# Kernel optimization log

Measured on AMD Instinct MI355X. Metric: run time of the kernel, lower is better.

The kernel has to match this reference:

```python
import jax, jax.numpy as jnp
import numpy as np
import math

INPUT_SIZE = 1024
OUTPUT_SIZE = 1024
QK_SIZE = 1024
B, S = 4, 2048


def setup_inputs() -> dict:
    key = jax.random.key(0)
    ks = jax.random.split(key, 7)
    scale = 1.0 / math.sqrt(INPUT_SIZE)
    return {
        "x": jax.random.normal(ks[0], (B, S, INPUT_SIZE), dtype=jnp.float32),
        "Wq": jax.random.uniform(ks[1], (QK_SIZE, INPUT_SIZE), minval=-scale, maxval=scale, dtype=jnp.float32),
        "bq": jax.random.uniform(ks[2], (QK_SIZE,), minval=-scale, maxval=scale, dtype=jnp.float32),
        "Wk": jax.random.uniform(ks[3], (QK_SIZE, INPUT_SIZE), minval=-scale, maxval=scale, dtype=jnp.float32),
        "bk": jax.random.uniform(ks[4], (QK_SIZE,), minval=-scale, maxval=scale, dtype=jnp.float32),
        "Wv": jax.random.uniform(ks[5], (OUTPUT_SIZE, INPUT_SIZE), minval=-scale, maxval=scale, dtype=jnp.float32),
        "bv": jax.random.uniform(ks[6], (OUTPUT_SIZE,), minval=-scale, maxval=scale, dtype=jnp.float32),
    }


def reference(x, Wq, bq, Wk, bk, Wv, bv):
    # torch Linear: y = x @ W.T + b
    q = jnp.einsum('bsd,ed->bse', x, Wq) + bq  # [B,S,QK]
    k = jnp.einsum('bsd,ed->bse', x, Wk) + bk  # [B,S,QK]
    v = jnp.einsum('bsd,ed->bse', x, Wv) + bv  # [B,S,OUT]
    inv_sqrt_d = 1.0 / math.sqrt(QK_SIZE)
    scores = jnp.einsum('bqe,bke->bqk', q, k) * inv_sqrt_d  # [B,S,S]
    attn = jax.nn.softmax(scores, axis=-1)
    return jnp.einsum('bqk,bko->bqo', attn, v)  # [B,S,OUT]
```

## Files before the change

### kernel.cpp

```cpp
#include <hip/hip_runtime.h>
#include <stdint.h>

typedef unsigned short u16;
typedef __attribute__((ext_vector_type(8))) __bf16 bf16x8;
typedef __attribute__((ext_vector_type(4))) float f32x4;

__device__ __forceinline__ u16 f2bf(float f) {
    union { float f; uint32_t u; } v; v.f = f;
    uint32_t r = (v.u + 0x7FFFu + ((v.u >> 16) & 1u)) >> 16;
    return (u16)r;
}

__device__ __forceinline__ void lds_fence() {
    __asm__ volatile("s_waitcnt lgkmcnt(0)" ::: "memory");
}

#define BARRIER() __asm__ volatile("s_barrier" ::: "memory")
#define VMW(N)    __asm__ volatile("s_waitcnt vmcnt(" #N ")" ::: "memory")
#define SCHEDB()  __builtin_amdgcn_sched_barrier(0)

template<int MODE>
__global__ __launch_bounds__(512, 2) void gemm8(
    const u16* __restrict__ A, const u16* __restrict__ Bt,
    const float* __restrict__ b0, const float* __restrict__ b1, const float* __restrict__ b2,
    u16* __restrict__ o0, u16* __restrict__ o1, u16* __restrict__ o2,
    float* __restrict__ o3, float* __restrict__ lsum,
    int M, int N, int K, long sA, long sB, long sC, float scale)
{
    extern __shared__ __align__(16) u16 smem[];

    const int t = threadIdx.x;
    const int lane = t & 63;
    const int wave = t >> 6;
    const int wm = wave >> 2;
    const int wn = wave & 3;

    const int id = blockIdx.x;
    const int xcd = id & 7;
    const int s = id >> 3;
    int bm, bn;
    long bz;
    if (MODE == 0) {
        bm = (xcd * 4 + (s & 3)) * 256;
        bn = (s >> 2) * 256;
        bz = 0;
    } else if (MODE == 2) {
        bz = xcd >> 1;
        bm = ((xcd & 1) * 4 + (s & 3)) * 256;
        bn = (s >> 2) * 256;
    } else {
        bz = xcd >> 1;
        bm = ((xcd & 1) * 4 + (s & 3)) * 256;
        bn = (s >> 2) * 256;
    }

    const u16* Ab = A + bz * sA;
    const u16* Bb = Bt + bz * sB;

    f32x4 acc[8][4];
#pragma unroll
    for (int i = 0; i < 8; ++i)
#pragma unroll
        for (int j = 0; j < 4; ++j)
            acc[i][j] = (f32x4){0.f, 0.f, 0.f, 0.f};

    const int trow = t >> 2;
    const int gcol = ((t & 3) * 8) ^ ((trow & 8) << 1);
    const u16* aRow = Ab + (long)(bm + trow) * K + gcol;
    const u16* bRow = Bb + (long)(bn + trow) * K + gcol;

    auto stage = [&](int buf, int kt, int h, int isB) {
        const u16* g = (isB ? bRow : aRow) + (long)(h * 128) * K + kt * 64;
        u16* d = smem + t * 8 + buf * 32768 + isB * 16384 + h * 8192;
#pragma unroll
        for (int l = 0; l < 2; ++l)
            __builtin_amdgcn_global_load_lds(
                (const __attribute__((address_space(1))) void*)(g + l * 32),
                (__attribute__((address_space(3))) void*)(d + l * 4096), 16, 0, 0);
    };

    const int fm = lane & 15;
    const int fcol = ((lane >> 4) * 8) ^ ((fm & 8) << 1);
    const int aB = wm * 8192 + fm * 32 + fcol;
    const int bB = 16384 + (wn >> 1) * 8192 + (wn & 1) * 2048 + fm * 32 + fcol;

    bf16x8 fa[4][2], fb0[2][2], fb1[2][2];

#define RD_A(BUF, MH) do { \
    _Pragma("unroll") for (int mi = 0; mi < 4; ++mi) \
    _Pragma("unroll") for (int kh = 0; kh < 2; ++kh) \
        fa[mi][kh] = *(const bf16x8*)&smem[(BUF)*32768 + aB + kh*4096 + (MH)*2048 + mi*512]; \
} while (0)

#define RD_B(BUF, NH, DST) do { \
    _Pragma("unroll") for (int ni = 0; ni < 2; ++ni) \
    _Pragma("unroll") for (int kh = 0; kh < 2; ++kh) \
        DST[ni][kh] = *(const bf16x8*)&smem[(BUF)*32768 + bB + kh*4096 + (NH)*1024 + ni*512]; \
} while (0)

#define QUAD(MH, NH, FB) do { \
    __builtin_amdgcn_s_setprio(1); \
    _Pragma("unroll") for (int mi = 0; mi < 4; ++mi) \
    _Pragma("unroll") for (int ni = 0; ni < 2; ++ni) \
    _Pragma("unroll") for (int kh = 0; kh < 2; ++kh) \
        acc[(MH)*4+mi][(NH)*2+ni] = __builtin_amdgcn_mfma_f32_16x16x32_bf16( \
            fa[mi][kh], FB[ni][kh], acc[(MH)*4+mi][(NH)*2+ni], 0, 0, 0); \
    __builtin_amdgcn_s_setprio(0); \
} while (0)

    const int NT = K >> 6;
    const int NI = NT >> 1;

    stage(0, 0, 0, 0); stage(0, 0, 1, 0); stage(0, 0, 0, 1); stage(0, 0, 1, 1);
    stage(1, 1, 0, 1); stage(1, 1, 0, 0);
    VMW(4);
    BARRIER();

    for (int i = 0; i < NI; ++i) {
        const int knext = 2 * i + 1;
        int ktc = 2 * i + 2; if (ktc >= NT) ktc -= NT;
        const int ktd = ktc + 1;

        RD_A(0, 0); RD_B(0, 0, fb0);
        stage(1, knext, 1, 0);
        BARRIER(); SCHEDB();
        QUAD(0, 0, fb0);
        BARRIER();
        RD_B(0, 1, fb1);
        stage(1, knext, 1, 1);
        BARRIER(); SCHEDB();
        QUAD(0, 1, fb1);
        BARRIER();
        RD_A(0, 1);
        stage(0, ktc, 0, 1);
        BARRIER(); SCHEDB();
        QUAD(1, 1, fb1);
        BARRIER();
        stage(0, ktc, 0, 0);
        BARRIER(); SCHEDB();
        QUAD(1, 0, fb0);
        VMW(4);
        BARRIER();
        RD_A(1, 0); RD_B(1, 0, fb0);
        stage(0, ktc, 1, 0);
        BARRIER(); SCHEDB();
        QUAD(0, 0, fb0);
        BARRIER();
        RD_B(1, 1, fb1);
        stage(0, ktc, 1, 1);
        BARRIER(); SCHEDB();
        QUAD(0, 1, fb1);
        BARRIER();
        RD_A(1, 1);
        stage(1, ktd, 0, 1);
        BARRIER(); SCHEDB();
        QUAD(1, 1, fb1);
        BARRIER();
        stage(1, ktd, 0, 0);
        BARRIER(); SCHEDB();
        QUAD(1, 0, fb0);
        VMW(4);
        BARRIER();
    }

    VMW(0);
    BARRIER();

    const int cm = (lane >> 4) * 4;
    const int cn = lane & 15;
    u16* Ew = smem + wave * 8192;
    const int gmb = bm + wm * 128;
    const int cnb = bn + wn * 64;

    if (MODE == 3) {
        float* Fw = (float*)Ew;
#pragma unroll
        for (int p = 0; p < 4; ++p) {
            if (p) lds_fence();
#pragma unroll
            for (int m2 = 0; m2 < 2; ++m2) {
                const int mi = p * 2 + m2;
#pragma unroll
                for (int ni = 0; ni < 4; ++ni)
#pragma unroll
                    for (int r = 0; r < 4; ++r)
                        Fw[(m2 * 16 + cm + r) * 68 + ni * 16 + cn] = acc[mi][ni][r];
            }
#pragma unroll
            for (int it = 0; it < 8; ++it) {
                const int row = it * 4 + (lane >> 4);
                const int c4 = cn * 4;
                f32x4 w = *(const f32x4*)&Fw[row * 68 + c4];
                const int gm = gmb + p * 32 + row;
                const float inv = __builtin_amdgcn_rcpf(lsum[bz * 2048 + gm]);
                w[0] *= inv; w[1] *= inv; w[2] *= inv; w[3] *= inv;
                *(f32x4*)&o3[bz * sC + (long)gm * N + cnb + c4] = w;
            }
        }
    } else if (MODE == 0 && (bn >> 10) == 2) {
        const int ebase = (bn & 1023) + wn * 64;
        float bb[4];
#pragma unroll
        for (int ni = 0; ni < 4; ++ni) bb[ni] = b2[ebase + ni * 16 + cn];
        const long bgi = gmb >> 11;
        const int sbase = gmb & 2047;
#pragma unroll
        for (int p = 0; p < 2; ++p) {
            if (p) lds_fence();
#pragma unroll
            for (int m4 = 0; m4 < 4; ++m4) {
                const int mi = p * 4 + m4;
#pragma unroll
                for (int ni = 0; ni < 4; ++ni) {
                    ushort4 pk;
                    pk.x = f2bf(acc[mi][ni][0] + bb[ni]);
                    pk.y = f2bf(acc[mi][ni][1] + bb[ni]);
                    pk.z = f2bf(acc[mi][ni][2] + bb[ni]);
                    pk.w = f2bf(acc[mi][ni][3] + bb[ni]);
                    *(ushort4*)&Ew[(ni * 16 + cn) * 72 + m4 * 16 + cm] = pk;
                }
            }
#pragma unroll
            for (int it = 0; it < 8; ++it) {
                const int e = it * 8 + (lane >> 3);
                const int s8 = (lane & 7) * 8;
                const uint4 w = *(const uint4*)&Ew[e * 72 + s8];
                *(uint4*)&o2[(((bgi << 10) + ebase + e) << 11) + sbase + p * 64 + s8] = w;
            }
        }
    } else if (MODE == 0) {
        const int sec = bn >> 10;
        u16* C = sec ? o1 : o0;
        const float* bias = sec ? b1 : b0;
        const int ncol0 = (bn & 1023) + wn * 64;
        float bb[4];
#pragma unroll
        for (int ni = 0; ni < 4; ++ni) bb[ni] = bias[ncol0 + ni * 16 + cn];
#pragma unroll
        for (int p = 0; p < 2; ++p) {
            if (p) lds_fence();
#pragma unroll
            for (int m4 = 0; m4 < 4; ++m4) {
                const int mi = p * 4 + m4;
#pragma unroll
                for (int ni = 0; ni < 4; ++ni)
#pragma unroll
                    for (int r = 0; r < 4; ++r)
                        Ew[(m4 * 16 + cm + r) * 72 + ni * 16 + cn] = f2bf(acc[mi][ni][r] + bb[ni]);
            }
#pragma unroll
            for (int it = 0; it < 8; ++it) {
                const int row = it * 8 + (lane >> 3);
                const int c8 = (lane & 7) * 8;
                const uint4 w = *(const uint4*)&Ew[row * 72 + c8];
                *(uint4*)&C[(long)(gmb + p * 64 + row) * 1024 + ncol0 + c8] = w;
            }
        }
    } else {
#pragma unroll
        for (int mi = 0; mi < 8; ++mi)
#pragma unroll
            for (int ni = 0; ni < 4; ++ni)
#pragma unroll
                for (int r = 0; r < 4; ++r)
                    acc[mi][ni][r] = __expf(acc[mi][ni][r] * scale);
#pragma unroll
        for (int mi = 0; mi < 8; ++mi) {
#pragma unroll
            for (int r = 0; r < 4; ++r) {
                float sm = acc[mi][0][r] + acc[mi][1][r] + acc[mi][2][r] + acc[mi][3][r];
                sm += __shfl_xor(sm, 1);
                sm += __shfl_xor(sm, 2);
                sm += __shfl_xor(sm, 4);
                sm += __shfl_xor(sm, 8);
                if (cn == 0)
                    atomicAdd(&lsum[bz * 2048 + gmb + mi * 16 + cm + r], sm);
            }
        }
#pragma unroll
        for (int p = 0; p < 2; ++p) {
            if (p) lds_fence();
#pragma unroll
            for (int m4 = 0; m4 < 4; ++m4) {
                const int mi = p * 4 + m4;
#pragma unroll
                for (int ni = 0; ni < 4; ++ni)
#pragma unroll
                    for (int r = 0; r < 4; ++r)
                        Ew[(m4 * 16 + cm + r) * 72 + ni * 16 + cn] = f2bf(acc[mi][ni][r]);
            }
#pragma unroll
            for (int it = 0; it < 8; ++it) {
                const int row = it * 8 + (lane >> 3);
                const int c8 = (lane & 7) * 8;
                const uint4 w = *(const uint4*)&Ew[row * 72 + c8];
                *(uint4*)&o0[bz * sC + (long)(gmb + p * 64 + row) * N + cnb + c8] = w;
            }
        }
    }
}

#undef RD_A
#undef RD_B
#undef QUAD

__global__ __launch_bounds__(256) void cvt_all(
    const float* __restrict__ x, const float* __restrict__ wq,
    const float* __restrict__ wk, const float* __restrict__ wv,
    u16* __restrict__ xb, u16* __restrict__ wb, float* __restrict__ lsum)
{
    const int b = blockIdx.x;
    if (b >= 11264) {
        const long i = (long)(b - 11264) * 1024 + threadIdx.x * 4;
        *(f32x4*)(lsum + i) = (f32x4){0.f, 0.f, 0.f, 0.f};
        return;
    }
    const float* src; u16* dst; long base;
    if (b < 8192)       { src = x;  dst = xb;             base = (long)b * 1024; }
    else if (b < 9216)  { src = wq; dst = wb;             base = (long)(b - 8192) * 1024; }
    else if (b < 10240) { src = wk; dst = wb + (1 << 20); base = (long)(b - 9216) * 1024; }
    else                { src = wv; dst = wb + (2 << 20); base = (long)(b - 10240) * 1024; }
    const long i = base + threadIdx.x * 4;
    const f32x4 f = *(const f32x4*)(src + i);
    ushort4 o;
    o.x = f2bf(f[0]); o.y = f2bf(f[1]); o.z = f2bf(f[2]); o.w = f2bf(f[3]);
    *(ushort4*)(dst + i) = o;
}

extern "C" void kernel_launch(void* const* d_in, const int* in_sizes, int n_in,
                              void* d_out, int out_size, void* d_ws, size_t ws_size,
                              hipStream_t stream) {
    const float* x  = (const float*)d_in[0];
    const float* Wq = (const float*)d_in[1];
    const float* bq = (const float*)d_in[2];
    const float* Wk = (const float*)d_in[3];
    const float* bk = (const float*)d_in[4];
    const float* Wv = (const float*)d_in[5];
    const float* bv = (const float*)d_in[6];
    float* out = (float*)d_out;

    const int B = 4, S = 2048, D = 1024, E = 1024;
    const int M = B * S;
    const size_t LDS = 131072;

    u16* xb  = (u16*)d_ws;
    u16* wb  = xb  + (size_t)M * D;
    u16* qb  = wb  + (size_t)3 * E * D;
    u16* kb  = qb  + (size_t)M * E;
    u16* vbT = kb  + (size_t)M * E;
    u16* sb  = vbT + (size_t)M * E;
    float* lsum = (float*)(sb + (size_t)M * S);

    static bool attr_done = false;
    if (!attr_done) {
        (void)hipFuncSetAttribute((const void*)gemm8<0>, hipFuncAttributeMaxDynamicSharedMemorySize, (int)LDS);
        (void)hipFuncSetAttribute((const void*)gemm8<2>, hipFuncAttributeMaxDynamicSharedMemorySize, (int)LDS);
        (void)hipFuncSetAttribute((const void*)gemm8<3>, hipFuncAttributeMaxDynamicSharedMemorySize, (int)LDS);
        attr_done = true;
    }

    cvt_all<<<11272, 256, 0, stream>>>(x, Wq, Wk, Wv, xb, wb, lsum);

    dim3 blk(512);
    gemm8<0><<<384, blk, LDS, stream>>>(
        xb, wb, bq, bk, bv, qb, kb, vbT, nullptr, nullptr, M, 3 * E, D, 0, 0, 0, 1.f);
    gemm8<2><<<256, blk, LDS, stream>>>(
        qb, kb, nullptr, nullptr, nullptr, sb, nullptr, nullptr, nullptr, lsum,
        S, S, E, (long)S * E, (long)S * E, (long)S * S, 0.03125f);
    gemm8<3><<<128, blk, LDS, stream>>>(
        sb, vbT, nullptr, nullptr, nullptr, nullptr, nullptr, nullptr, out, lsum,
        S, E, S, (long)S * S, (long)E * S, (long)S * E, 1.f);
}
```

Before: 244.0 us.

## Halve N tile of P·V GEMM to 128 and double its grid

The final attention-times-V GEMM now uses 256x128 tiles instead of 256x256, launching 256 workgroups instead of 128. This fills more of the GPU's compute units on the third kernel, at the cost of re-reading the score matrix twice as often. The B staging, fragment reads and epilogue are adjusted for the narrower tile, and the vmcnt waits are retuned per mode. The compiler sched_barrier hints are removed and the raw s_barrier asm is replaced with the builtin, which changes how instructions may be scheduled in all modes.

```diff
diff --git a/kernel.cpp b/kernel.cpp
--- a/kernel.cpp
+++ b/kernel.cpp
@@ -15,9 +15,8 @@
     __asm__ volatile("s_waitcnt lgkmcnt(0)" ::: "memory");
 }
 
-#define BARRIER() __asm__ volatile("s_barrier" ::: "memory")
+#define BARRIER() __builtin_amdgcn_s_barrier()
 #define VMW(N)    __asm__ volatile("s_waitcnt vmcnt(" #N ")" ::: "memory")
-#define SCHEDB()  __builtin_amdgcn_sched_barrier(0)
 
 template<int MODE>
 __global__ __launch_bounds__(512, 2) void gemm8(
@@ -28,6 +27,9 @@
     int M, int N, int K, long sA, long sB, long sC, float scale)
 {
     extern __shared__ __align__(16) u16 smem[];
+    constexpr int NIR = (MODE == 3) ? 1 : 2;
+    constexpr int NJ  = (MODE == 3) ? 2 : 4;
+    constexpr int NHS = (MODE == 3) ? 512 : 1024;
 
     const int t = threadIdx.x;
     const int lane = t & 63;
@@ -51,17 +53,17 @@
     } else {
         bz = xcd >> 1;
         bm = ((xcd & 1) * 4 + (s & 3)) * 256;
-        bn = (s >> 2) * 256;
+        bn = (s >> 2) * 128;
     }
 
     const u16* Ab = A + bz * sA;
     const u16* Bb = Bt + bz * sB;
 
-    f32x4 acc[8][4];
+    f32x4 acc[8][NJ];
 #pragma unroll
     for (int i = 0; i < 8; ++i)
 #pragma unroll
-        for (int j = 0; j < 4; ++j)
+        for (int j = 0; j < NJ; ++j)
             acc[i][j] = (f32x4){0.f, 0.f, 0.f, 0.f};
 
     const int trow = t >> 2;
@@ -82,9 +84,11 @@
     const int fm = lane & 15;
     const int fcol = ((lane >> 4) * 8) ^ ((fm & 8) << 1);
     const int aB = wm * 8192 + fm * 32 + fcol;
-    const int bB = 16384 + (wn >> 1) * 8192 + (wn & 1) * 2048 + fm * 32 + fcol;
-
-    bf16x8 fa[4][2], fb0[2][2], fb1[2][2];
+    const int bB = (MODE == 3)
+        ? 16384 + wn * 1024 + fm * 32 + fcol
+        : 16384 + (wn >> 1) * 8192 + (wn & 1) * 2048 + fm * 32 + fcol;
+
+    bf16x8 fa[4][2], fb0[NIR][2], fb1[NIR][2];
 
 #define RD_A(BUF, MH) do { \
     _Pragma("unroll") for (int mi = 0; mi < 4; ++mi) \
@@ -93,27 +97,28 @@
 } while (0)
 
 #define RD_B(BUF, NH, DST) do { \
-    _Pragma("unroll") for (int ni = 0; ni < 2; ++ni) \
+    _Pragma("unroll") for (int ni = 0; ni < NIR; ++ni) \
     _Pragma("unroll") for (int kh = 0; kh < 2; ++kh) \
-        DST[ni][kh] = *(const bf16x8*)&smem[(BUF)*32768 + bB + kh*4096 + (NH)*1024 + ni*512]; \
+        DST[ni][kh] = *(const bf16x8*)&smem[(BUF)*32768 + bB + kh*4096 + (NH)*NHS + ni*512]; \
 } while (0)
 
 #define QUAD(MH, NH, FB) do { \
     __builtin_amdgcn_s_setprio(1); \
     _Pragma("unroll") for (int mi = 0; mi < 4; ++mi) \
-    _Pragma("unroll") for (int ni = 0; ni < 2; ++ni) \
+    _Pragma("unroll") for (int ni = 0; ni < NIR; ++ni) \
     _Pragma("unroll") for (int kh = 0; kh < 2; ++kh) \
-        acc[(MH)*4+mi][(NH)*2+ni] = __builtin_amdgcn_mfma_f32_16x16x32_bf16( \
-            fa[mi][kh], FB[ni][kh], acc[(MH)*4+mi][(NH)*2+ni], 0, 0, 0); \
+        acc[(MH)*4+mi][(NH)*NIR+ni] = __builtin_amdgcn_mfma_f32_16x16x32_bf16( \
+            fa[mi][kh], FB[ni][kh], acc[(MH)*4+mi][(NH)*NIR+ni], 0, 0, 0); \
     __builtin_amdgcn_s_setprio(0); \
 } while (0)
 
     const int NT = K >> 6;
     const int NI = NT >> 1;
 
-    stage(0, 0, 0, 0); stage(0, 0, 1, 0); stage(0, 0, 0, 1); stage(0, 0, 1, 1);
+    stage(0, 0, 0, 0); stage(0, 0, 1, 0); stage(0, 0, 0, 1);
+    if (MODE != 3) stage(0, 0, 1, 1);
     stage(1, 1, 0, 1); stage(1, 1, 0, 0);
-    VMW(4);
+    if (MODE == 3) { VMW(4); } else { VMW(6); }
     BARRIER();
 
     for (int i = 0; i < NI; ++i) {
@@ -123,43 +128,45 @@
 
         RD_A(0, 0); RD_B(0, 0, fb0);
         stage(1, knext, 1, 0);
-        BARRIER(); SCHEDB();
+        BARRIER();
         QUAD(0, 0, fb0);
+        if (MODE != 3) VMW(6);
         BARRIER();
         RD_B(0, 1, fb1);
-        stage(1, knext, 1, 1);
-        BARRIER(); SCHEDB();
+        if (MODE != 3) stage(1, knext, 1, 1);
+        BARRIER();
         QUAD(0, 1, fb1);
         BARRIER();
         RD_A(0, 1);
         stage(0, ktc, 0, 1);
-        BARRIER(); SCHEDB();
+        BARRIER();
         QUAD(1, 1, fb1);
         BARRIER();
         stage(0, ktc, 0, 0);
-        BARRIER(); SCHEDB();
+        BARRIER();
         QUAD(1, 0, fb0);
-        VMW(4);
+        if (MODE == 3) { VMW(4); } else { VMW(6); }
         BARRIER();
         RD_A(1, 0); RD_B(1, 0, fb0);
         stage(0, ktc, 1, 0);
-        BARRIER(); SCHEDB();
+        BARRIER();
         QUAD(0, 0, fb0);
+        if (MODE != 3) VMW(6);
         BARRIER();
         RD_B(1, 1, fb1);
-        stage(0, ktc, 1, 1);
-        BARRIER(); SCHEDB();
+        if (MODE != 3) stage(0, ktc, 1, 1);
+        BARRIER();
         QUAD(0, 1, fb1);
         BARRIER();
         RD_A(1, 1);
         stage(1, ktd, 0, 1);
-        BARRIER(); SCHEDB();
+        BARRIER();
         QUAD(1, 1, fb1);
         BARRIER();
         stage(1, ktd, 0, 0);
-        BARRIER(); SCHEDB();
+        BARRIER();
         QUAD(1, 0, fb0);
-        VMW(4);
+        if (MODE == 3) { VMW(4); } else { VMW(6); }
         BARRIER();
     }
 
@@ -170,10 +177,10 @@
     const int cn = lane & 15;
     u16* Ew = smem + wave * 8192;
     const int gmb = bm + wm * 128;
-    const int cnb = bn + wn * 64;
-
-    if (MODE == 3) {
+
+    if constexpr (MODE == 3) {
         float* Fw = (float*)Ew;
+        const int cnb3 = bn + wn * 32;
 #pragma unroll
         for (int p = 0; p < 4; ++p) {
             if (p) lds_fence();
@@ -181,20 +188,20 @@
             for (int m2 = 0; m2 < 2; ++m2) {
                 const int mi = p * 2 + m2;
 #pragma unroll
-                for (int ni = 0; ni < 4; ++ni)
+                for (int ni = 0; ni < 2; ++ni)
 #pragma unroll
                     for (int r = 0; r < 4; ++r)
-                        Fw[(m2 * 16 + cm + r) * 68 + ni * 16 + cn] = acc[mi][ni][r];
-            }
-#pragma unroll
-            for (int it = 0; it < 8; ++it) {
-                const int row = it * 4 + (lane >> 4);
-                const int c4 = cn * 4;
-                f32x4 w = *(const f32x4*)&Fw[row * 68 + c4];
+                        Fw[(m2 * 16 + cm + r) * 36 + ni * 16 + cn] = acc[mi][ni][r];
+            }
+#pragma unroll
+            for (int it = 0; it < 4; ++it) {
+                const int row = it * 8 + (lane >> 3);
+                const int c4 = (lane & 7) * 4;
+                f32x4 w = *(const f32x4*)&Fw[row * 36 + c4];
                 const int gm = gmb + p * 32 + row;
                 const float inv = __builtin_amdgcn_rcpf(lsum[bz * 2048 + gm]);
                 w[0] *= inv; w[1] *= inv; w[2] *= inv; w[3] *= inv;
-                *(f32x4*)&o3[bz * sC + (long)gm * N + cnb + c4] = w;
+                *(f32x4*)&o3[bz * sC + (long)gm * N + cnb3 + c4] = w;
             }
         }
     } else if (MODE == 0 && (bn >> 10) == 2) {
@@ -257,6 +264,7 @@
             }
         }
     } else {
+        const int cnb = bn + wn * 64;
 #pragma unroll
         for (int mi = 0; mi < 8; ++mi)
 #pragma unroll
@@ -367,7 +375,7 @@
     gemm8<2><<<256, blk, LDS, stream>>>(
         qb, kb, nullptr, nullptr, nullptr, sb, nullptr, nullptr, nullptr, lsum,
         S, S, E, (long)S * E, (long)S * E, (long)S * S, 0.03125f);
-    gemm8<3><<<128, blk, LDS, stream>>>(
+    gemm8<3><<<256, blk, LDS, stream>>>(
         sb, vbT, nullptr, nullptr, nullptr, nullptr, nullptr, nullptr, out, lsum,
         S, E, S, (long)S * S, (long)E * S, (long)S * E, 1.f);
 }
```

After: 231.2 us. -5.3%, faster.
